# Optimization experiments

Measured on AMD Instinct MI355X. Metric: run time of the kernel, lower is better.

## Reference

```python
import jax, jax.numpy as jnp
import numpy as np
from jax import lax

DN = ('NCHW', 'OIHW', 'NCHW')  # torch layout


def softplus(a):
    # torch code: log(1 + exp(clamp(a, min=-88)))
    return jnp.log(1.0 + jnp.exp(jnp.maximum(a, -88.0)))


def _conv(x, w):
    return lax.conv_general_dilated(x, w, window_strides=(1, 1), padding='VALID',
                                    dimension_numbers=DN)


def setup_inputs() -> dict:
    key = jax.random.key(0)
    k1, k2, k3, k4, k5 = jax.random.split(key, 5)
    B, C, O, H, Wd, K = 16, 128, 256, 96, 96, 5
    mu_x = jax.random.normal(k1, (B, C, H, Wd), dtype=jnp.float32)
    sigma_x = jax.random.uniform(k2, (B, C, H, Wd), dtype=jnp.float32)
    # xavier-ish scale for conv weight
    W = jax.random.normal(k3, (O, C, K, K), dtype=jnp.float32) * (1.0 / np.sqrt(C * K * K))
    bias = jax.random.normal(k4, (O,), dtype=jnp.float32)
    w_sigma = jax.random.uniform(k5, (O, 1), dtype=jnp.float32) * 5.0
    return {"mu_x": mu_x, "sigma_x": sigma_x, "W": W, "bias": bias, "w_sigma": w_sigma}


def reference(mu_x, sigma_x, W, bias, w_sigma):
    # mu path: ordinary conv
    mu_y = _conv(mu_x, W) + bias[None, :, None, None]

    # sigma path. In the original, softplus(w_sigma) is repeated across the
    # C*kh*kw unfold dim, so the first and third terms reduce to a per-output
    # scalar times a sum over each receptive field -> conv with a ones kernel.
    # The second term is a conv of sigma_x with W**2. This is mathematically
    # identical to the unfold + batched-matmul chain, without materializing
    # the im2col tensors.
    O, C, kh, kw = W.shape
    sp = softplus(w_sigma)[:, 0]                      # [O]
    ones_k = jnp.ones((1, C, kh, kw), dtype=W.dtype)  # sum over receptive field
    s_sum = _conv(sigma_x, ones_k)                    # [B,1,H',W'] : sum_k unfold(sigma_x)
    m2_sum = _conv(mu_x * mu_x, ones_k)               # [B,1,H',W'] : sum_k unfold(mu_x)^2
    w2_term = _conv(sigma_x, W * W)                   # [B,O,H',W']
    sigma_y = (sp[None, :, None, None] * (s_sum + m2_sum) + w2_term) * 0.001
    return (mu_y, sigma_y)
```

## Files before the change

kernel.cpp:

```cpp
#include <hip/hip_runtime.h>
#include <stdint.h>

typedef __attribute__((ext_vector_type(8))) short bf16x8_t;
typedef __attribute__((ext_vector_type(4))) float f32x4_t;
typedef __attribute__((ext_vector_type(4))) unsigned int u32x4_t;

#define B_ 16
#define C_ 128
#define O_ 256
#define H_ 96
#define W_ 96
#define HO_ 92
#define WO_ 92

#define XMU_OFF 0UL
#define XSG_OFF 37748736UL
#define WP_OFF  75497472UL
#define W2P_OFF 77135872UL
#define SP_OFF  78774272UL
#define T_OFF   78775296UL
#define S_OFF   79365120UL

__device__ __forceinline__ unsigned short f2bf(float f) {
  unsigned u = __float_as_uint(f);
  u += 0x7fffu + ((u >> 16) & 1u);
  return (unsigned short)(u >> 16);
}

#if defined(__has_builtin)
#if __has_builtin(__builtin_amdgcn_global_load_lds)
#define USE_GLL 1
#endif
#endif
#ifndef USE_GLL
#define USE_GLL 0
#endif

__device__ __forceinline__ void stage16(unsigned short* lds_base, const unsigned short* gp, int lane) {
#if USE_GLL
  __builtin_amdgcn_global_load_lds(
      (const __attribute__((address_space(1))) void*)gp,
      (__attribute__((address_space(3))) void*)lds_base, 16, 0, 0);
#else
  *((u32x4_t*)lds_base + lane) = *(const u32x4_t*)gp;
#endif
}


__global__ void k_sp(const float* __restrict__ wsig, float* __restrict__ sp) {
  int o = threadIdx.x;
  float a = fmaxf(wsig[o], -88.0f);
  sp[o] = log1pf(expf(a));
}

__global__ void k_zero(float* __restrict__ t) {
  t[blockIdx.x * 256 + threadIdx.x] = 0.0f;
}

__global__ void k_packw(const float* __restrict__ W, unsigned short* __restrict__ Wp,
                        unsigned short* __restrict__ W2p) {
  int gid = blockIdx.x * 256 + threadIdx.x;
  int ci  = gid & 31;
  int o   = (gid >> 5) & 255;
  int cc4 = (gid >> 13) & 3;
  int t25 = gid >> 15;
  int c = cc4 * 32 + ci;
  float w = W[((size_t)o * 128 + c) * 25 + t25];
  Wp[gid]  = f2bf(w);
  W2p[gid] = f2bf(w * w);
}

__global__ void k_cast(const float* __restrict__ mu, const float* __restrict__ sg,
                       unsigned short* __restrict__ Xmu, unsigned short* __restrict__ Xsg,
                       float* __restrict__ t) {
  __shared__ float sl[128 * 97];
  __shared__ float part[192];
  int bh = blockIdx.x;
  int b = bh / 96, h = bh - b * 96;
  const int is_mu = (blockIdx.y == 0);
  const float* src = is_mu ? mu : sg;
  unsigned short* dst = is_mu ? Xmu : Xsg;
  int tid = threadIdx.x;
#pragma unroll
  for (int i = 0; i < 12; ++i) {
    int f4 = tid + i * 256;
    int c = f4 / 24, w4 = f4 - c * 24;
    f32x4_t v = *(const f32x4_t*)(src + (((size_t)b * 128 + c) * 96 + h) * 96 + w4 * 4);
    float* s = sl + c * 97 + w4 * 4;
    s[0] = v.x; s[1] = v.y; s[2] = v.z; s[3] = v.w;
  }
  __syncthreads();
  unsigned short* drow = dst + ((size_t)b * 96 + h) * (size_t)(96 * 128);
#pragma unroll
  for (int i = 0; i < 6; ++i) {
    int chunk = tid + i * 256;
    int w = chunk >> 4;
    int c0 = (chunk & 15) * 8;
    u32x4_t pk;
#pragma unroll
    for (int e = 0; e < 4; ++e) {
      unsigned lo = f2bf(sl[(c0 + 2 * e) * 97 + w]);
      unsigned hi = f2bf(sl[(c0 + 2 * e + 1) * 97 + w]);
      pk[e] = lo | (hi << 16);
    }
    *(u32x4_t*)(drow + (size_t)w * 128 + c0) = pk;
  }
  if (tid < 192) {
    int half = tid / 96, w = tid - half * 96;
    float s = 0.f;
#pragma unroll 4
    for (int c = half * 64; c < half * 64 + 64; ++c) {
      float v = sl[c * 97 + w];
      s += is_mu ? v * v : v;
    }
    part[tid] = s;
  }
  __syncthreads();
  if (tid < 96)
    atomicAdd(&t[((size_t)b * 96 + h) * 96 + tid], part[tid] + part[96 + tid]);
}

__global__ void k_S(const float* __restrict__ t, float* __restrict__ S) {
  int gid = blockIdx.x * 256 + threadIdx.x;
  if (gid >= 135424) return;
  int b = gid / 8464;
  int r = gid - b * 8464;
  int y = r / 92;
  int x = r - y * 92;
  const float* tp = t + (size_t)b * 9216 + (size_t)y * 96 + x;
  float s = 0.f;
#pragma unroll
  for (int kh = 0; kh < 5; ++kh) {
    const float* row = tp + kh * 96;
#pragma unroll
    for (int kw = 0; kw < 5; ++kw) s += row[kw];
  }
  S[gid] = s;
}

__global__ __launch_bounds__(256, 2) void k_conv(
    const unsigned short* __restrict__ Xmu, const unsigned short* __restrict__ Xsg,
    const unsigned short* __restrict__ Wp,  const unsigned short* __restrict__ W2p,
    const float* __restrict__ bias, const float* __restrict__ sp,
    const float* __restrict__ Sb, float* __restrict__ out) {
  __shared__ char smem[25600];
  unsigned short* Alds = (unsigned short*)smem;

  const int mode = blockIdx.y;
  const unsigned short* X   = mode ? Xsg : Xmu;
  const unsigned short* Wt0 = mode ? W2p : Wp;

  const int bid0 = blockIdx.x;
  const int bid  = (bid0 & 7) * 184 + (bid0 >> 3);
  const int b = bid / HO_;
  const int y = bid - b * HO_;

  const int tid  = threadIdx.x;
  const int wv   = tid >> 6;
  const int lane = tid & 63;
  const int l15  = lane & 15;
  const int g4   = lane >> 4;

  const int p_st = lane >> 4;
  const int q_st = lane & 15;

  f32x4_t acc[6][4];
#pragma unroll
  for (int im = 0; im < 6; ++im)
#pragma unroll
    for (int in = 0; in < 4; ++in)
      acc[im][in] = (f32x4_t)0.0f;

  const int bo = (wv * 64 + l15) * 32 + g4 * 8;

  for (int kh = 0; kh < 5; ++kh) {
    const unsigned short* Xrow = X + ((size_t)(b * H_ + y + kh) * W_) * C_;
    __syncthreads();
#pragma unroll
    for (int jj = 0; jj < 6; ++jj) {
      const int j = wv + jj * 4;
      const int p = j * 4 + p_st;
      const int c0 = (q_st ^ (p & 15)) * 8;
      stage16(Alds + j * 512, Xrow + p * C_ + c0, lane);
    }
    __syncthreads();
#pragma unroll
    for (int kw = 0; kw < 5; ++kw) {
      const unsigned short* Wt = Wt0 + (size_t)(kh * 5 + kw) * 32768;
      int prow[6], pxor[6];
#pragma unroll
      for (int im = 0; im < 6; ++im) {
        int p = im * 16 + l15 + kw;
        p = p < 95 ? p : 95;
        prow[im] = p << 7;
        pxor[im] = p & 15;
      }
#pragma unroll
      for (int cc = 0; cc < 4; ++cc) {
        bf16x8_t bfr[4];
#pragma unroll
        for (int in = 0; in < 4; ++in)
          bfr[in] = *(const bf16x8_t*)(Wt + cc * 8192 + in * 512 + bo);
        bf16x8_t af[6];
        const int cl = cc * 4 + g4;
#pragma unroll
        for (int im = 0; im < 6; ++im)
          af[im] = *(const bf16x8_t*)(Alds + prow[im] + ((cl ^ pxor[im]) << 3));
        __builtin_amdgcn_s_setprio(1);
#pragma unroll
        for (int im = 0; im < 6; ++im)
#pragma unroll
          for (int in = 0; in < 4; ++in)
            acc[im][in] = __builtin_amdgcn_mfma_f32_16x16x32_bf16(af[im], bfr[in], acc[im][in], 0, 0, 0);
        __builtin_amdgcn_s_setprio(0);
      }
    }
  }

  float* epi = (float*)smem + wv * 1600;
  const size_t outbase = (size_t)mode * ((size_t)B_ * O_ * HO_ * WO_);
  const int orow = lane >> 2, seg = lane & 3;
  const float* Srow = Sb + ((size_t)b * HO_ + y) * WO_;
#pragma unroll
  for (int in = 0; in < 4; ++in) {
    __syncthreads();
#pragma unroll
    for (int im = 0; im < 6; ++im)
#pragma unroll
      for (int r = 0; r < 4; ++r)
        epi[l15 * 100 + im * 16 + g4 * 4 + r] = acc[im][in][r];
    __syncthreads();
    const int o = wv * 64 + in * 16 + orow;
    const float scal = mode ? sp[o] : bias[o];
    const float* erow = epi + orow * 100;
    float* optr = out + outbase + ((size_t)(b * O_ + o) * HO_ + y) * WO_;
#pragma unroll
    for (int jq = 0; jq < 6; ++jq) {
      int q = jq * 4 + seg;
      if (q < 23) {
        f32x4_t v = *(const f32x4_t*)(erow + q * 4);
        int x = q * 4;
        if (mode) {
          f32x4_t s4 = *(const f32x4_t*)(Srow + x);
          v = (scal * s4 + v) * 0.001f;
        } else {
          v = v + scal;
        }
        *(f32x4_t*)(optr + x) = v;
      }
    }
  }
}

extern "C" void kernel_launch(void* const* d_in, const int* in_sizes, int n_in,
                              void* d_out, int out_size, void* d_ws, size_t ws_size,
                              hipStream_t stream) {
  const float* mu   = (const float*)d_in[0];
  const float* sg   = (const float*)d_in[1];
  const float* W    = (const float*)d_in[2];
  const float* bias = (const float*)d_in[3];
  const float* wsig = (const float*)d_in[4];
  float* out = (float*)d_out;
  char* ws = (char*)d_ws;

  unsigned short* Xmu = (unsigned short*)(ws + XMU_OFF);
  unsigned short* Xsg = (unsigned short*)(ws + XSG_OFF);
  unsigned short* Wp  = (unsigned short*)(ws + WP_OFF);
  unsigned short* W2p = (unsigned short*)(ws + W2P_OFF);
  float* sp = (float*)(ws + SP_OFF);
  float* tb = (float*)(ws + T_OFF);
  float* Sb = (float*)(ws + S_OFF);

  k_sp<<<1, 256, 0, stream>>>(wsig, sp);
  k_zero<<<576, 256, 0, stream>>>(tb);
  k_packw<<<3200, 256, 0, stream>>>(W, Wp, W2p);
  k_cast<<<dim3(1536, 2), 256, 0, stream>>>(mu, sg, Xmu, Xsg, tb);
  k_S<<<529, 256, 0, stream>>>(tb, Sb);
  k_conv<<<dim3(B_ * HO_, 2), 256, 0, stream>>>(Xmu, Xsg, Wp, W2p, bias, sp, Sb, out);
}
```

Before: 738.5 us.

## Fuse small prep kernels into packw and conv epilogue, cut launches from six to three

```diff
diff --git a/kernel.cpp b/kernel.cpp
--- a/kernel.cpp
+++ b/kernel.cpp
@@ -47,27 +47,36 @@
 }
 
 
-__global__ void k_sp(const float* __restrict__ wsig, float* __restrict__ sp) {
-  int o = threadIdx.x;
-  float a = fmaxf(wsig[o], -88.0f);
-  sp[o] = log1pf(expf(a));
-}
-
-__global__ void k_zero(float* __restrict__ t) {
-  t[blockIdx.x * 256 + threadIdx.x] = 0.0f;
-}
-
 __global__ void k_packw(const float* __restrict__ W, unsigned short* __restrict__ Wp,
-                        unsigned short* __restrict__ W2p) {
-  int gid = blockIdx.x * 256 + threadIdx.x;
-  int ci  = gid & 31;
-  int o   = (gid >> 5) & 255;
-  int cc4 = (gid >> 13) & 3;
-  int t25 = gid >> 15;
-  int c = cc4 * 32 + ci;
-  float w = W[((size_t)o * 128 + c) * 25 + t25];
-  Wp[gid]  = f2bf(w);
-  W2p[gid] = f2bf(w * w);
+                        unsigned short* __restrict__ W2p, float* __restrict__ t) {
+  __shared__ float wl[6400];
+  const int tid = threadIdx.x;
+  {
+    int idx = blockIdx.x * 256 + tid;
+#pragma unroll
+    for (int k = 0; k < 5; ++k) {
+      int j = idx + k * 32768;
+      if (j < 147456) t[j] = 0.0f;
+    }
+  }
+  const int o0 = blockIdx.x * 2;
+  const float* Wo = W + (size_t)o0 * 3200;
+#pragma unroll
+  for (int i = 0; i < 25; ++i)
+    wl[i * 256 + tid] = Wo[i * 256 + tid];
+  __syncthreads();
+  const int o1 = tid >> 7;
+  const int c  = tid & 127;
+  const int cc4 = c >> 5, ci = c & 31;
+  const float* src = wl + o1 * 3200 + c * 25;
+  const size_t dbase = (size_t)cc4 * 8192 + (size_t)(o0 + o1) * 32 + ci;
+#pragma unroll
+  for (int t25 = 0; t25 < 25; ++t25) {
+    float w = src[t25];
+    size_t a = (size_t)t25 * 32768 + dbase;
+    Wp[a]  = f2bf(w);
+    W2p[a] = f2bf(w * w);
+  }
 }
 
 __global__ void k_cast(const float* __restrict__ mu, const float* __restrict__ sg,
@@ -120,30 +129,13 @@
     atomicAdd(&t[((size_t)b * 96 + h) * 96 + tid], part[tid] + part[96 + tid]);
 }
 
-__global__ void k_S(const float* __restrict__ t, float* __restrict__ S) {
-  int gid = blockIdx.x * 256 + threadIdx.x;
-  if (gid >= 135424) return;
-  int b = gid / 8464;
-  int r = gid - b * 8464;
-  int y = r / 92;
-  int x = r - y * 92;
-  const float* tp = t + (size_t)b * 9216 + (size_t)y * 96 + x;
-  float s = 0.f;
-#pragma unroll
-  for (int kh = 0; kh < 5; ++kh) {
-    const float* row = tp + kh * 96;
-#pragma unroll
-    for (int kw = 0; kw < 5; ++kw) s += row[kw];
-  }
-  S[gid] = s;
-}
-
 __global__ __launch_bounds__(256, 2) void k_conv(
     const unsigned short* __restrict__ Xmu, const unsigned short* __restrict__ Xsg,
     const unsigned short* __restrict__ Wp,  const unsigned short* __restrict__ W2p,
-    const float* __restrict__ bias, const float* __restrict__ sp,
-    const float* __restrict__ Sb, float* __restrict__ out) {
+    const float* __restrict__ bias, const float* __restrict__ wsig,
+    const float* __restrict__ tb, float* __restrict__ out) {
   __shared__ char smem[25600];
+  __shared__ __align__(16) float SrowL[96];
   unsigned short* Alds = (unsigned short*)smem;
 
   const int mode = blockIdx.y;
@@ -160,6 +152,18 @@
   const int lane = tid & 63;
   const int l15  = lane & 15;
   const int g4   = lane >> 4;
+
+  if (mode && tid < WO_) {
+    const float* tp = tb + (size_t)b * 9216 + (size_t)y * 96 + tid;
+    float s = 0.f;
+#pragma unroll
+    for (int kh = 0; kh < 5; ++kh) {
+      const float* row = tp + kh * 96;
+#pragma unroll
+      for (int kw = 0; kw < 5; ++kw) s += row[kw];
+    }
+    SrowL[tid] = s;
+  }
 
   const int p_st = lane >> 4;
   const int q_st = lane & 15;
@@ -220,7 +224,6 @@
   float* epi = (float*)smem + wv * 1600;
   const size_t outbase = (size_t)mode * ((size_t)B_ * O_ * HO_ * WO_);
   const int orow = lane >> 2, seg = lane & 3;
-  const float* Srow = Sb + ((size_t)b * HO_ + y) * WO_;
 #pragma unroll
   for (int in = 0; in < 4; ++in) {
     __syncthreads();
@@ -231,7 +234,7 @@
         epi[l15 * 100 + im * 16 + g4 * 4 + r] = acc[im][in][r];
     __syncthreads();
     const int o = wv * 64 + in * 16 + orow;
-    const float scal = mode ? sp[o] : bias[o];
+    const float scal = mode ? log1pf(expf(fmaxf(wsig[o], -88.0f))) : bias[o];
     const float* erow = epi + orow * 100;
     float* optr = out + outbase + ((size_t)(b * O_ + o) * HO_ + y) * WO_;
 #pragma unroll
@@ -241,7 +244,7 @@
         f32x4_t v = *(const f32x4_t*)(erow + q * 4);
         int x = q * 4;
         if (mode) {
-          f32x4_t s4 = *(const f32x4_t*)(Srow + x);
+          f32x4_t s4 = *(const f32x4_t*)(SrowL + x);
           v = (scal * s4 + v) * 0.001f;
         } else {
           v = v + scal;
@@ -267,14 +270,9 @@
   unsigned short* Xsg = (unsigned short*)(ws + XSG_OFF);
   unsigned short* Wp  = (unsigned short*)(ws + WP_OFF);
   unsigned short* W2p = (unsigned short*)(ws + W2P_OFF);
-  float* sp = (float*)(ws + SP_OFF);
   float* tb = (float*)(ws + T_OFF);
-  float* Sb = (float*)(ws + S_OFF);
-
-  k_sp<<<1, 256, 0, stream>>>(wsig, sp);
-  k_zero<<<576, 256, 0, stream>>>(tb);
-  k_packw<<<3200, 256, 0, stream>>>(W, Wp, W2p);
+
+  k_packw<<<128, 256, 0, stream>>>(W, Wp, W2p, tb);
   k_cast<<<dim3(1536, 2), 256, 0, stream>>>(mu, sg, Xmu, Xsg, tb);
-  k_S<<<529, 256, 0, stream>>>(tb, Sb);
-  k_conv<<<dim3(B_ * HO_, 2), 256, 0, stream>>>(Xmu, Xsg, Wp, W2p, bias, sp, Sb, out);
-}
+  k_conv<<<dim3(B_ * HO_, 2), 256, 0, stream>>>(Xmu, Xsg, Wp, W2p, bias, wsig, tb, out);
+}
```

Result: no change. 738.7 us (+0.0%).
